# Optimization experiments

Measured on AMD Instinct MI355X. Metric: run time of the kernel, lower is better.

The kernel has to match this reference:

```python
import jax, jax.numpy as jnp
import numpy as np

N_NODES = 50000
GAMMA = -0.5
ZETA = 1.1
DEBUG_VAR = 1e-07


def setup_inputs() -> dict:
    key = jax.random.key(0)
    ks = jax.random.split(key, 8)
    N, E, D, H = N_NODES, 800000, 256, 128
    s = 0.05
    return {
        "x": jax.random.normal(ks[0], (N, D), jnp.float32),
        "W_nb": jax.random.normal(ks[1], (D, H), jnp.float32) * s,
        "b_nb": jnp.zeros((H,), jnp.float32),
        "W_self": jax.random.normal(ks[2], (D, H), jnp.float32) * s,
        "b_self": jnp.zeros((H,), jnp.float32),
        "W_att": jax.random.normal(ks[3], (2 * H, 1), jnp.float32) * s,
        "b_att": jnp.zeros((1,), jnp.float32),
        "values": jax.random.uniform(ks[4], (E,), jnp.float32),
        "noise": jax.random.uniform(ks[5], (E, 1), jnp.float32),
        "row": jax.random.randint(ks[6], (E,), 0, N, jnp.int32),
        "col": jax.random.randint(ks[7], (E,), 0, N, jnp.int32),
    }


def reference(x, W_nb, b_nb, W_self, b_self, W_att, b_att, values, noise, row, col):
    # edge gather + tiny attention MLP
    f1 = jax.nn.relu(x[row] @ W_nb + b_nb)      # [E, H]
    f2 = jax.nn.relu(x[col] @ W_self + b_self)  # [E, H]
    log_alpha = jnp.concatenate([f1, f2], axis=1) @ W_att + b_att  # [E, 1]

    # hard-concrete sample (training=True), beta=1.0
    u = noise + DEBUG_VAR
    gate = jax.nn.sigmoid(jnp.log(u) - jnp.log(1.0 - u) + log_alpha)
    mask = jnp.clip(gate * (ZETA - GAMMA) + GAMMA, 0.0, 1.0)[:, 0]  # [E]

    masked_values = values * mask

    # degree-normalized scatter: rowsum then symmetric D^{-1/2} A D^{-1/2}
    rowsum = jax.ops.segment_sum(masked_values, row, num_segments=N_NODES) + 1e-10
    d_inv_sqrt = jnp.power(rowsum, -0.5)
    d_inv_sqrt = jnp.where(jnp.isinf(d_inv_sqrt), 0.0, d_inv_sqrt)

    norm_values = masked_values * d_inv_sqrt[row] * d_inv_sqrt[col]  # [E]
    return norm_values
```

## Files before the change

kernel.cpp:

```cpp
#include <hip/hip_runtime.h>
#include <hip/hip_bf16.h>

typedef __attribute__((ext_vector_type(8))) short bf16x8;
typedef __attribute__((ext_vector_type(4))) float f32x4;

#define D_DIM 256
#define H_DIM 128
#define QSH 12544
#define NSL 64
#define NMAXL (4 * QSH)

__device__ inline ushort f2bf(float f) {
    union { float f; unsigned u; } a; a.f = f;
    unsigned r = a.u + 0x7fffu + ((a.u >> 16) & 1u);
    return (ushort)(r >> 16);
}
__device__ inline float bf2f(unsigned hi16) {
    union { unsigned u; float f; } a; a.u = hi16 << 16;
    return a.f;
}

__global__ void k0_init(const float* __restrict__ W_nb, const float* __restrict__ W_self,
                        ushort* __restrict__ Wt, float* __restrict__ dis, int N, int init_dis) {
    int i = blockIdx.x * 256 + threadIdx.x;
    if (i < 2 * H_DIM * D_DIM) {
        int j    = i & 7;
        int lane = (i >> 3) & 63;
        int ks   = (i >> 9) & 7;
        int ni   = (i >> 12) & 3;
        int cg   = i >> 14;
        int li   = lane & 15;
        int grp  = lane >> 4;
        int h    = (cg & 1) * 64 + ni * 16 + li;
        int k    = ks * 32 + grp * 8 + j;
        const float* W = (cg >> 1) ? W_self : W_nb;
        Wt[i] = f2bf(W[k * H_DIM + h]);
    }
    if (init_dis && i < N) dis[i] = 1e-10f;
}

__global__ __launch_bounds__(512, 2) void k1_gemm(
    const float* __restrict__ x, const ushort* __restrict__ Wt,
    const float* __restrict__ b_nb, const float* __restrict__ b_self,
    const float* __restrict__ W_att,
    float* __restrict__ g_nb, float* __restrict__ g_self, int N, int ntiles)
{
    __shared__ __align__(16) ushort A_lds[64][264];
    __shared__ float part[2][2][64];

    const int t    = threadIdx.x;
    const int lane = t & 63;
    const int w    = t >> 6;
    const int rh   = w >> 2;
    const int cg   = w & 3;
    const int br   = cg >> 1;
    const int ch   = cg & 1;
    const int li   = lane & 15;
    const int grp  = lane >> 4;

    float bias[4], aw[4];
    #pragma unroll
    for (int ni = 0; ni < 4; ni++) {
        int hh = ch * 64 + ni * 16 + li;
        bias[ni] = br ? b_self[hh] : b_nb[hh];
        aw[ni]   = W_att[br * H_DIM + hh];
    }

    bf16x8 Bf[4][8];
    #pragma unroll
    for (int ni = 0; ni < 4; ni++)
        #pragma unroll
        for (int ks = 0; ks < 8; ks++)
            Bf[ni][ks] = *reinterpret_cast<const bf16x8*>(
                Wt + (((size_t)(cg * 4 + ni) * 8 + ks) << 9) + lane * 8);

    const int sr = t >> 3;
    const int sc = t & 7;

    for (int rt = blockIdx.x; rt < ntiles; rt += gridDim.x) {
        const int row0 = rt * 64;

        __syncthreads();
        {
            const int gr = row0 + sr;
            const bool v = gr < N;
            const float4* src = reinterpret_cast<const float4*>(x + (size_t)gr * D_DIM);
            #pragma unroll
            for (int j = 0; j < 8; j++) {
                int c4 = sc + j * 8;
                ushort4 o;
                if (v) {
                    float4 f = src[c4];
                    o.x = f2bf(f.x); o.y = f2bf(f.y); o.z = f2bf(f.z); o.w = f2bf(f.w);
                } else { o.x = 0; o.y = 0; o.z = 0; o.w = 0; }
                *reinterpret_cast<ushort4*>(&A_lds[sr][c4 * 4]) = o;
            }
        }
        __syncthreads();

        f32x4 acc[2][4];
        #pragma unroll
        for (int mi = 0; mi < 2; mi++)
            #pragma unroll
            for (int ni = 0; ni < 4; ni++) acc[mi][ni] = f32x4{0.f, 0.f, 0.f, 0.f};

        #pragma unroll
        for (int ks = 0; ks < 8; ks++) {
            bf16x8 af0 = *reinterpret_cast<const bf16x8*>(&A_lds[rh * 32 + li][ks * 32 + grp * 8]);
            bf16x8 af1 = *reinterpret_cast<const bf16x8*>(&A_lds[rh * 32 + 16 + li][ks * 32 + grp * 8]);
            #pragma unroll
            for (int ni = 0; ni < 4; ni++) {
                acc[0][ni] = __builtin_amdgcn_mfma_f32_16x16x32_bf16(af0, Bf[ni][ks], acc[0][ni], 0, 0, 0);
                acc[1][ni] = __builtin_amdgcn_mfma_f32_16x16x32_bf16(af1, Bf[ni][ks], acc[1][ni], 0, 0, 0);
            }
        }

        float p[2][4];
        #pragma unroll
        for (int mi = 0; mi < 2; mi++)
            #pragma unroll
            for (int r4 = 0; r4 < 4; r4++) p[mi][r4] = 0.f;
        #pragma unroll
        for (int ni = 0; ni < 4; ni++)
            #pragma unroll
            for (int mi = 0; mi < 2; mi++)
                #pragma unroll
                for (int r4 = 0; r4 < 4; r4++) {
                    float y = acc[mi][ni][r4] + bias[ni];
                    y = y > 0.f ? y : 0.f;
                    p[mi][r4] += y * aw[ni];
                }
        #pragma unroll
        for (int mi = 0; mi < 2; mi++)
            #pragma unroll
            for (int r4 = 0; r4 < 4; r4++) {
                float v = p[mi][r4];
                #pragma unroll
                for (int m = 1; m < 16; m <<= 1) v += __shfl_xor(v, m);
                if (li == 0)
                    part[br][ch][rh * 32 + mi * 16 + grp * 4 + r4] = v;
            }
        __syncthreads();

        if (t < 128) {
            int b_ = t >> 6, lr = t & 63;
            int gr = row0 + lr;
            if (gr < N) {
                float val = part[b_][0][lr] + part[b_][1][lr];
                if (b_) g_self[gr] = val; else g_nb[gr] = val;
            }
        }
    }
}

__global__ __launch_bounds__(256) void k2a_gate(
    const int* __restrict__ row, const int* __restrict__ col,
    const float* __restrict__ values, const float* __restrict__ noise,
    const float* __restrict__ g_nb, const float* __restrict__ g_self,
    const float* __restrict__ b_att, unsigned* __restrict__ pk, int E)
{
    int i = (blockIdx.x * 256 + threadIdx.x) * 4;
    if (i >= E) return;
    const float ba = b_att[0];
    if (i + 3 < E) {
        int4   r4 = *reinterpret_cast<const int4*>(row + i);
        int4   c4 = *reinterpret_cast<const int4*>(col + i);
        float4 v4 = *reinterpret_cast<const float4*>(values + i);
        float4 u4 = *reinterpret_cast<const float4*>(noise + i);
        int   rr[4] = { r4.x, r4.y, r4.z, r4.w };
        int   cc[4] = { c4.x, c4.y, c4.z, c4.w };
        float vv[4] = { v4.x, v4.y, v4.z, v4.w };
        float uu[4] = { u4.x, u4.y, u4.z, u4.w };
        float gn[4], gs[4];
        #pragma unroll
        for (int j = 0; j < 4; j++) { gn[j] = g_nb[rr[j]]; gs[j] = g_self[cc[j]]; }
        unsigned pkv[4];
        #pragma unroll
        for (int j = 0; j < 4; j++) {
            float u    = uu[j] + 1e-7f;
            float la   = gn[j] + gs[j] + ba;
            float gate = u / (u + (1.f - u) * __expf(-la));
            float mask = fminf(fmaxf(gate * 1.6f - 0.5f, 0.f), 1.f);
            pkv[j] = ((unsigned)rr[j] << 16) | (unsigned)f2bf(vv[j] * mask);
        }
        *reinterpret_cast<uint4*>(pk + i) = make_uint4(pkv[0], pkv[1], pkv[2], pkv[3]);
    } else {
        for (int j = 0; j < 4 && i + j < E; j++) {
            int e = i + j;
            int   r = row[e];
            float u    = noise[e] + 1e-7f;
            float la   = g_nb[r] + g_self[col[e]] + ba;
            float gate = u / (u + (1.f - u) * __expf(-la));
            float mask = fminf(fmaxf(gate * 1.6f - 0.5f, 0.f), 1.f);
            pk[e] = ((unsigned)r << 16) | (unsigned)f2bf(values[e] * mask);
        }
    }
}

__global__ __launch_bounds__(1024) void k2q_scatter(
    const unsigned* __restrict__ pk, ushort* __restrict__ priv, int E, int ES)
{
    __shared__ float acc[QSH];
    const int s  = blockIdx.x >> 2;
    const int q  = blockIdx.x & 3;
    const int t  = threadIdx.x;
    const int lo = q * QSH;

    for (int i = t; i < QSH; i += 1024) acc[i] = 0.f;
    __syncthreads();

    const int base = s * ES;
    int end = base + ES; if (end > E) end = E;

    int i = base + t * 4;
    for (; i + 3 < end; i += 4096) {
        uint4 p4 = *reinterpret_cast<const uint4*>(pk + i);
        unsigned p; int d; float m;
        p = p4.x; d = (int)(p >> 16) - lo; m = bf2f(p & 0xffffu);
        if ((unsigned)d < (unsigned)QSH && m != 0.f) atomicAdd(&acc[d], m);
        p = p4.y; d = (int)(p >> 16) - lo; m = bf2f(p & 0xffffu);
        if ((unsigned)d < (unsigned)QSH && m != 0.f) atomicAdd(&acc[d], m);
        p = p4.z; d = (int)(p >> 16) - lo; m = bf2f(p & 0xffffu);
        if ((unsigned)d < (unsigned)QSH && m != 0.f) atomicAdd(&acc[d], m);
        p = p4.w; d = (int)(p >> 16) - lo; m = bf2f(p & 0xffffu);
        if ((unsigned)d < (unsigned)QSH && m != 0.f) atomicAdd(&acc[d], m);
    }
    for (; i < end; i++) {
        unsigned p = pk[i];
        int d = (int)(p >> 16) - lo;
        float m = bf2f(p & 0xffffu);
        if ((unsigned)d < (unsigned)QSH && m != 0.f) atomicAdd(&acc[d], m);
    }
    __syncthreads();

    ushort* dst = priv + (size_t)s * (4 * QSH) + lo;
    for (int j = t * 2; j < QSH; j += 2048) {
        unsigned pkk = (unsigned)f2bf(acc[j]) | ((unsigned)f2bf(acc[j + 1]) << 16);
        *reinterpret_cast<unsigned*>(dst + j) = pkk;
    }
}

__global__ __launch_bounds__(256) void k2c_reduce(
    const ushort* __restrict__ priv, ushort* __restrict__ disb, int N)
{
    int n0 = (blockIdx.x * 256 + threadIdx.x) * 2;
    if (n0 >= N) return;
    float s0 = 1e-10f, s1 = 1e-10f;
    for (int p = 0; p < NSL; p++) {
        unsigned v = *reinterpret_cast<const unsigned*>(priv + (size_t)p * (4 * QSH) + n0);
        s0 += bf2f(v & 0xffffu);
        s1 += bf2f(v >> 16);
    }
    unsigned o = (unsigned)f2bf(rsqrtf(s0)) | ((unsigned)f2bf(rsqrtf(s1)) << 16);
    *reinterpret_cast<unsigned*>(disb + n0) = o;
}

__global__ __launch_bounds__(1024) void k3_edge2_lds(
    const unsigned* __restrict__ pk, const int* __restrict__ col,
    float* __restrict__ out, const ushort* __restrict__ disb,
    int Npad2, int E, int EB)
{
    __shared__ ushort ldis[NMAXL];
    const int t = threadIdx.x;
    {
        const unsigned* src = reinterpret_cast<const unsigned*>(disb);
        unsigned* dst = reinterpret_cast<unsigned*>(ldis);
        const int nw = Npad2 >> 1;
        for (int i = t; i < nw; i += 1024) dst[i] = src[i];
    }
    __syncthreads();

    const int base = blockIdx.x * EB;
    int end = base + EB; if (end > E) end = E;

    int i = base + t * 4;
    for (; i + 3 < end; i += 4096) {
        uint4 p4 = *reinterpret_cast<const uint4*>(pk + i);
        int4  c4 = *reinterpret_cast<const int4*>(col + i);
        float4 o;
        o.x = bf2f(p4.x & 0xffffu) * bf2f(ldis[p4.x >> 16]) * bf2f(ldis[c4.x]);
        o.y = bf2f(p4.y & 0xffffu) * bf2f(ldis[p4.y >> 16]) * bf2f(ldis[c4.y]);
        o.z = bf2f(p4.z & 0xffffu) * bf2f(ldis[p4.z >> 16]) * bf2f(ldis[c4.z]);
        o.w = bf2f(p4.w & 0xffffu) * bf2f(ldis[p4.w >> 16]) * bf2f(ldis[c4.w]);
        *reinterpret_cast<float4*>(out + i) = o;
    }
    for (; i < end; i++) {
        unsigned p = pk[i];
        out[i] = bf2f(p & 0xffffu) * bf2f(ldis[p >> 16]) * bf2f(ldis[col[i]]);
    }
}

__global__ __launch_bounds__(256) void k2_atomic_fb(
    const int* __restrict__ row, const int* __restrict__ col,
    const float* __restrict__ values, const float* __restrict__ noise,
    const float* __restrict__ g_nb, const float* __restrict__ g_self,
    const float* __restrict__ b_att,
    float* __restrict__ out, float* __restrict__ dis, int E)
{
    int e = blockIdx.x * 256 + threadIdx.x;
    if (e >= E) return;
    int   r = row[e], c = col[e];
    float u = noise[e] + 1e-7f;
    float la = g_nb[r] + g_self[c] + b_att[0];
    float gate = u / (u + (1.f - u) * __expf(-la));
    float mask = fminf(fmaxf(gate * 1.6f - 0.5f, 0.f), 1.f);
    float m = values[e] * mask;
    out[e] = m;
    if (m != 0.f) atomicAdd(&dis[r], m);
}
__global__ __launch_bounds__(256) void k2c_rsqrt_fb(float* __restrict__ dis, int N)
{
    int n = blockIdx.x * 256 + threadIdx.x;
    if (n < N) dis[n] = rsqrtf(dis[n]);
}
__global__ __launch_bounds__(256) void k3_edge2_fb(
    const int* __restrict__ row, const int* __restrict__ col,
    float* __restrict__ out, const float* __restrict__ dis, int E)
{
    int e = blockIdx.x * 256 + threadIdx.x;
    if (e >= E) return;
    out[e] = out[e] * dis[row[e]] * dis[col[e]];
}

extern "C" void kernel_launch(void* const* d_in, const int* in_sizes, int n_in,
                              void* d_out, int out_size, void* d_ws, size_t ws_size,
                              hipStream_t stream) {
    const float* x      = (const float*)d_in[0];
    const float* W_nb   = (const float*)d_in[1];
    const float* b_nb   = (const float*)d_in[2];
    const float* W_self = (const float*)d_in[3];
    const float* b_self = (const float*)d_in[4];
    const float* W_att  = (const float*)d_in[5];
    const float* b_att  = (const float*)d_in[6];
    const float* values = (const float*)d_in[7];
    const float* noise  = (const float*)d_in[8];
    const int*   row    = (const int*)d_in[9];
    const int*   col    = (const int*)d_in[10];

    const int N = in_sizes[0] / D_DIM;
    const int E = in_sizes[7];
    float* out = (float*)d_out;

    char* ws = (char*)d_ws;
    ushort* Wt     = (ushort*)ws;
    float*  g_nb   = (float*)(ws + 131072);
    float*  g_self = g_nb + N;
    float*  dis    = g_self + N;
    ushort* disb   = (ushort*)dis;
    ushort* priv   = (ushort*)(dis + N);
    size_t pk_off  = 131072 + (size_t)3 * N * 4 + (size_t)NSL * NMAXL * 2;
    pk_off = (pk_off + 15) & ~(size_t)15;
    unsigned* pk   = (unsigned*)(ws + pk_off);

    const int Npad2 = (N + 1) & ~1;
    int ES = ((E + NSL - 1) / NSL + 3) & ~3;
    size_t need = pk_off + (size_t)E * 4;
    bool lds_path = (N <= NMAXL) && (need <= ws_size);

    int init_n = 2 * H_DIM * D_DIM;
    if (N > init_n) init_n = N;
    k0_init<<<(init_n + 255) / 256, 256, 0, stream>>>(W_nb, W_self, Wt, dis, N, lds_path ? 0 : 1);

    const int ntiles = (N + 63) / 64;
    k1_gemm<<<256, 512, 0, stream>>>(x, Wt, b_nb, b_self, W_att, g_nb, g_self, N, ntiles);

    if (lds_path) {
        int eb4 = ((E + 3) / 4 + 255) / 256;
        k2a_gate<<<eb4, 256, 0, stream>>>(row, col, values, noise, g_nb, g_self,
                                          b_att, pk, E);
        k2q_scatter<<<NSL * 4, 1024, 0, stream>>>(pk, priv, E, ES);
        k2c_reduce<<<((N + 1) / 2 + 255) / 256, 256, 0, stream>>>(priv, disb, N);
        int EB = ((E + 255) / 256 + 3) & ~3;
        k3_edge2_lds<<<256, 1024, 0, stream>>>(pk, col, out, disb, Npad2, E, EB);
    } else {
        k2_atomic_fb<<<(E + 255) / 256, 256, 0, stream>>>(row, col, values, noise,
                                                          g_nb, g_self, b_att, out, dis, E);
        k2c_rsqrt_fb<<<(N + 255) / 256, 256, 0, stream>>>(dis, N);
        k3_edge2_fb<<<(E + 255) / 256, 256, 0, stream>>>(row, col, out, dis, E);
    }
}
```

Measured before the change: 58.05 us.

## Load GEMM A-fragments directly from global into registers, drop LDS staging

The node GEMM kernel stops staging 64-row tiles of x into shared memory. Each of four waves now loads its own 16-row fragment straight from global memory into registers, converting to bf16 on the fly. Tiles shrink to 16 rows, blocks to 256 threads, and the grid grows to 512 blocks. This removes the LDS write/read and one barrier per tile. In exchange, all four waves read the same x rows (redundant global/L2 traffic), and each lane's loads are strided 32-byte chunks that coalesce less well.

Measured after the change: 64.48 us. 1.11x slower.

```diff
diff --git a/kernel.cpp b/kernel.cpp
--- a/kernel.cpp
+++ b/kernel.cpp
@@ -39,20 +39,17 @@
     if (init_dis && i < N) dis[i] = 1e-10f;
 }
 
-__global__ __launch_bounds__(512, 2) void k1_gemm(
+__global__ __launch_bounds__(256, 2) void k1_gemm(
     const float* __restrict__ x, const ushort* __restrict__ Wt,
     const float* __restrict__ b_nb, const float* __restrict__ b_self,
     const float* __restrict__ W_att,
     float* __restrict__ g_nb, float* __restrict__ g_self, int N, int ntiles)
 {
-    __shared__ __align__(16) ushort A_lds[64][264];
-    __shared__ float part[2][2][64];
+    __shared__ float part[4][16];
 
     const int t    = threadIdx.x;
     const int lane = t & 63;
-    const int w    = t >> 6;
-    const int rh   = w >> 2;
-    const int cg   = w & 3;
+    const int cg   = t >> 6;
     const int br   = cg >> 1;
     const int ch   = cg & 1;
     const int li   = lane & 15;
@@ -74,82 +71,66 @@
             Bf[ni][ks] = *reinterpret_cast<const bf16x8*>(
                 Wt + (((size_t)(cg * 4 + ni) * 8 + ks) << 9) + lane * 8);
 
-    const int sr = t >> 3;
-    const int sc = t & 7;
-
     for (int rt = blockIdx.x; rt < ntiles; rt += gridDim.x) {
-        const int row0 = rt * 64;
-
-        __syncthreads();
-        {
-            const int gr = row0 + sr;
-            const bool v = gr < N;
-            const float4* src = reinterpret_cast<const float4*>(x + (size_t)gr * D_DIM);
+        const int row0 = rt * 16;
+        const int gr   = row0 + li;
+        const bool v   = gr < N;
+        const float* xr = x + (size_t)gr * D_DIM + grp * 8;
+
+        union { bf16x8 v8; ushort u[8]; } af[8];
+        #pragma unroll
+        for (int ks = 0; ks < 8; ks++) {
+            float4 a0, a1;
+            if (v) {
+                a0 = *reinterpret_cast<const float4*>(xr + ks * 32);
+                a1 = *reinterpret_cast<const float4*>(xr + ks * 32 + 4);
+            } else {
+                a0 = make_float4(0.f, 0.f, 0.f, 0.f);
+                a1 = a0;
+            }
+            af[ks].u[0] = f2bf(a0.x); af[ks].u[1] = f2bf(a0.y);
+            af[ks].u[2] = f2bf(a0.z); af[ks].u[3] = f2bf(a0.w);
+            af[ks].u[4] = f2bf(a1.x); af[ks].u[5] = f2bf(a1.y);
+            af[ks].u[6] = f2bf(a1.z); af[ks].u[7] = f2bf(a1.w);
+        }
+
+        f32x4 acc[4];
+        #pragma unroll
+        for (int ni = 0; ni < 4; ni++) acc[ni] = f32x4{0.f, 0.f, 0.f, 0.f};
+        #pragma unroll
+        for (int ks = 0; ks < 8; ks++)
             #pragma unroll
-            for (int j = 0; j < 8; j++) {
-                int c4 = sc + j * 8;
-                ushort4 o;
-                if (v) {
-                    float4 f = src[c4];
-                    o.x = f2bf(f.x); o.y = f2bf(f.y); o.z = f2bf(f.z); o.w = f2bf(f.w);
-                } else { o.x = 0; o.y = 0; o.z = 0; o.w = 0; }
-                *reinterpret_cast<ushort4*>(&A_lds[sr][c4 * 4]) = o;
-            }
-        }
-        __syncthreads();
-
-        f32x4 acc[2][4];
-        #pragma unroll
-        for (int mi = 0; mi < 2; mi++)
-            #pragma unroll
-            for (int ni = 0; ni < 4; ni++) acc[mi][ni] = f32x4{0.f, 0.f, 0.f, 0.f};
-
-        #pragma unroll
-        for (int ks = 0; ks < 8; ks++) {
-            bf16x8 af0 = *reinterpret_cast<const bf16x8*>(&A_lds[rh * 32 + li][ks * 32 + grp * 8]);
-            bf16x8 af1 = *reinterpret_cast<const bf16x8*>(&A_lds[rh * 32 + 16 + li][ks * 32 + grp * 8]);
+            for (int ni = 0; ni < 4; ni++)
+                acc[ni] = __builtin_amdgcn_mfma_f32_16x16x32_bf16(af[ks].v8, Bf[ni][ks], acc[ni], 0, 0, 0);
+
+        float p[4];
+        #pragma unroll
+        for (int r4 = 0; r4 < 4; r4++) {
+            float s = 0.f;
             #pragma unroll
             for (int ni = 0; ni < 4; ni++) {
-                acc[0][ni] = __builtin_amdgcn_mfma_f32_16x16x32_bf16(af0, Bf[ni][ks], acc[0][ni], 0, 0, 0);
-                acc[1][ni] = __builtin_amdgcn_mfma_f32_16x16x32_bf16(af1, Bf[ni][ks], acc[1][ni], 0, 0, 0);
+                float y = acc[ni][r4] + bias[ni];
+                y = y > 0.f ? y : 0.f;
+                s += y * aw[ni];
             }
-        }
-
-        float p[2][4];
-        #pragma unroll
-        for (int mi = 0; mi < 2; mi++)
             #pragma unroll
-            for (int r4 = 0; r4 < 4; r4++) p[mi][r4] = 0.f;
-        #pragma unroll
-        for (int ni = 0; ni < 4; ni++)
+            for (int m = 1; m < 16; m <<= 1) s += __shfl_xor(s, m);
+            p[r4] = s;
+        }
+        if (li == 0) {
             #pragma unroll
-            for (int mi = 0; mi < 2; mi++)
-                #pragma unroll
-                for (int r4 = 0; r4 < 4; r4++) {
-                    float y = acc[mi][ni][r4] + bias[ni];
-                    y = y > 0.f ? y : 0.f;
-                    p[mi][r4] += y * aw[ni];
-                }
-        #pragma unroll
-        for (int mi = 0; mi < 2; mi++)
-            #pragma unroll
-            for (int r4 = 0; r4 < 4; r4++) {
-                float v = p[mi][r4];
-                #pragma unroll
-                for (int m = 1; m < 16; m <<= 1) v += __shfl_xor(v, m);
-                if (li == 0)
-                    part[br][ch][rh * 32 + mi * 16 + grp * 4 + r4] = v;
+            for (int r4 = 0; r4 < 4; r4++) part[cg][grp * 4 + r4] = p[r4];
+        }
+        __syncthreads();
+        if (t < 32) {
+            int node = t & 15, b_ = t >> 4;
+            int g2 = row0 + node;
+            if (g2 < N) {
+                float val = part[b_ * 2][node] + part[b_ * 2 + 1][node];
+                if (b_) g_self[g2] = val; else g_nb[g2] = val;
             }
+        }
         __syncthreads();
-
-        if (t < 128) {
-            int b_ = t >> 6, lr = t & 63;
-            int gr = row0 + lr;
-            if (gr < N) {
-                float val = part[b_][0][lr] + part[b_][1][lr];
-                if (b_) g_self[gr] = val; else g_nb[gr] = val;
-            }
-        }
     }
 }
 
@@ -361,8 +342,9 @@
     if (N > init_n) init_n = N;
     k0_init<<<(init_n + 255) / 256, 256, 0, stream>>>(W_nb, W_self, Wt, dis, N, lds_path ? 0 : 1);
 
-    const int ntiles = (N + 63) / 64;
-    k1_gemm<<<256, 512, 0, stream>>>(x, Wt, b_nb, b_self, W_att, g_nb, g_self, N, ntiles);
+    const int ntiles16 = (N + 15) / 16;
+    int k1grid = ntiles16 < 512 ? ntiles16 : 512;
+    k1_gemm<<<k1grid, 256, 0, stream>>>(x, Wt, b_nb, b_self, W_att, g_nb, g_self, N, ntiles16);
 
     if (lds_path) {
         int eb4 = ((E + 3) / 4 + 255) / 256;
```

## Pre-convert x to MFMA-swizzled bf16 and stage weights in LDS for GEMM

Applied to the files above, without the earlier changes.

The init kernel now also converts x to bf16, writing it in a layout that lets each lane load its MFMA A-fragments straight from global memory. A new GEMM kernel keeps one branch's transposed weights in XOR-swizzled LDS, splits the nb and self branches across alternating blocks, and computes 32-row tiles without staging x through LDS. The aim is to cut the per-tile LDS staging, conversion and barrier cost in the GEMM. The price is an extra bf16 copy of x written to and re-read from global memory (and read by both branch blocks), plus a larger workspace requirement.

New measurement: 67.30 us. +15.9%, slower.

```diff
diff --git a/kernel.cpp b/kernel.cpp
--- a/kernel.cpp
+++ b/kernel.cpp
@@ -20,26 +20,134 @@
     return a.f;
 }
 
-__global__ void k0_init(const float* __restrict__ W_nb, const float* __restrict__ W_self,
-                        ushort* __restrict__ Wt, float* __restrict__ dis, int N, int init_dis) {
+__global__ void k0_init(const float* __restrict__ x,
+                        const float* __restrict__ W_nb, const float* __restrict__ W_self,
+                        ushort* __restrict__ Wt, ushort* __restrict__ xbf,
+                        float* __restrict__ dis, int N, int init_dis, int do_xbf) {
     int i = blockIdx.x * 256 + threadIdx.x;
+    if (do_xbf && i < N * 32) {
+        int n     = i >> 5;
+        int kbase = (i & 31) * 8;
+        const float4* s = reinterpret_cast<const float4*>(x + (size_t)n * D_DIM + kbase);
+        float4 a = s[0], b = s[1];
+        uint4 o;
+        o.x = (unsigned)f2bf(a.x) | ((unsigned)f2bf(a.y) << 16);
+        o.y = (unsigned)f2bf(a.z) | ((unsigned)f2bf(a.w) << 16);
+        o.z = (unsigned)f2bf(b.x) | ((unsigned)f2bf(b.y) << 16);
+        o.w = (unsigned)f2bf(b.z) | ((unsigned)f2bf(b.w) << 16);
+        int T    = n >> 4;
+        int ks   = (i >> 2) & 7;
+        int l    = (i & 3) * 16 + (n & 15);
+        size_t word = ((size_t)T * 8 + ks) * 64 + l;
+        *reinterpret_cast<uint4*>(xbf + word * 8) = o;
+    }
     if (i < 2 * H_DIM * D_DIM) {
-        int j    = i & 7;
-        int lane = (i >> 3) & 63;
-        int ks   = (i >> 9) & 7;
-        int ni   = (i >> 12) & 3;
-        int cg   = i >> 14;
-        int li   = lane & 15;
-        int grp  = lane >> 4;
-        int h    = (cg & 1) * 64 + ni * 16 + li;
-        int k    = ks * 32 + grp * 8 + j;
-        const float* W = (cg >> 1) ? W_self : W_nb;
-        Wt[i] = f2bf(W[k * H_DIM + h]);
+        int sel = i >> 15;
+        int r   = i & 32767;
+        int k   = r >> 7;
+        int h   = r & 127;
+        const float* W = sel ? W_self : W_nb;
+        Wt[(sel * H_DIM + h) * D_DIM + k] = f2bf(W[k * H_DIM + h]);
     }
     if (init_dis && i < N) dis[i] = 1e-10f;
 }
 
-__global__ __launch_bounds__(512, 2) void k1_gemm(
+__global__ __launch_bounds__(256, 2) void k1_ldsb(
+    const ushort* __restrict__ xbf, const ushort* __restrict__ Wt,
+    const float* __restrict__ b_nb, const float* __restrict__ b_self,
+    const float* __restrict__ W_att,
+    float* __restrict__ g_nb, float* __restrict__ g_self,
+    int N, int nt16, int nt32)
+{
+    __shared__ ushort Bl[128 * 256];
+    __shared__ float part[4][32];
+
+    const int t    = threadIdx.x;
+    const int lane = t & 63;
+    const int w    = t >> 6;
+    const int li   = lane & 15;
+    const int grp  = lane >> 4;
+    const int cls  = blockIdx.x & 1;
+
+    {
+        const ushort* Wtg = Wt + (size_t)cls * H_DIM * D_DIM;
+        for (int q = t; q < 4096; q += 256) {
+            int row = q >> 5, c = q & 31;
+            uint4 v = *reinterpret_cast<const uint4*>(Wtg + row * 256 + c * 8);
+            *reinterpret_cast<uint4*>(&Bl[row * 256 + ((c ^ (row & 31)) << 3)]) = v;
+        }
+    }
+
+    float bias[2], aw[2];
+    #pragma unroll
+    for (int ni2 = 0; ni2 < 2; ni2++) {
+        int hl = w * 32 + ni2 * 16 + li;
+        bias[ni2] = cls ? b_self[hl] : b_nb[hl];
+        aw[ni2]   = W_att[cls * H_DIM + hl];
+    }
+    __syncthreads();
+
+    const int G  = gridDim.x >> 1;
+    const int r0 = w * 32 + li;
+    const int r1 = r0 + 16;
+
+    for (int T = blockIdx.x >> 1; T < nt32; T += G) {
+        bf16x8 af[2][8];
+        #pragma unroll
+        for (int mi = 0; mi < 2; mi++) {
+            int t16 = 2 * T + mi;
+            if (t16 < nt16) {
+                #pragma unroll
+                for (int ks = 0; ks < 8; ks++)
+                    af[mi][ks] = *reinterpret_cast<const bf16x8*>(
+                        xbf + (((size_t)t16 * 8 + ks) * 64 + lane) * 8);
+            } else {
+                #pragma unroll
+                for (int ks = 0; ks < 8; ks++) af[mi][ks] = bf16x8{0,0,0,0,0,0,0,0};
+            }
+        }
+
+        f32x4 acc[2][2];
+        #pragma unroll
+        for (int mi = 0; mi < 2; mi++)
+            #pragma unroll
+            for (int ni2 = 0; ni2 < 2; ni2++) acc[mi][ni2] = f32x4{0.f, 0.f, 0.f, 0.f};
+
+        #pragma unroll
+        for (int ks = 0; ks < 8; ks++) {
+            int c = ks * 4 + grp;
+            bf16x8 b0 = *reinterpret_cast<const bf16x8*>(&Bl[r0 * 256 + ((c ^ (r0 & 31)) << 3)]);
+            bf16x8 b1 = *reinterpret_cast<const bf16x8*>(&Bl[r1 * 256 + ((c ^ (r1 & 31)) << 3)]);
+            acc[0][0] = __builtin_amdgcn_mfma_f32_16x16x32_bf16(af[0][ks], b0, acc[0][0], 0, 0, 0);
+            acc[1][0] = __builtin_amdgcn_mfma_f32_16x16x32_bf16(af[1][ks], b0, acc[1][0], 0, 0, 0);
+            acc[0][1] = __builtin_amdgcn_mfma_f32_16x16x32_bf16(af[0][ks], b1, acc[0][1], 0, 0, 0);
+            acc[1][1] = __builtin_amdgcn_mfma_f32_16x16x32_bf16(af[1][ks], b1, acc[1][1], 0, 0, 0);
+        }
+
+        #pragma unroll
+        for (int mi = 0; mi < 2; mi++)
+            #pragma unroll
+            for (int r4 = 0; r4 < 4; r4++) {
+                float y0 = acc[mi][0][r4] + bias[0];
+                float y1 = acc[mi][1][r4] + bias[1];
+                y0 = y0 > 0.f ? y0 : 0.f;
+                y1 = y1 > 0.f ? y1 : 0.f;
+                float s = y0 * aw[0] + y1 * aw[1];
+                #pragma unroll
+                for (int m = 1; m < 16; m <<= 1) s += __shfl_xor(s, m);
+                if (li == 0) part[w][mi * 16 + grp * 4 + r4] = s;
+            }
+        __syncthreads();
+        if (t < 32) {
+            float val = part[0][t] + part[1][t] + part[2][t] + part[3][t];
+            int ng = T * 32 + t;
+            if (ng < N) (cls ? g_self : g_nb)[ng] = val;
+        }
+        __syncthreads();
+    }
+}
+
+__global__ __launch_bounds__(512, 2) void k1_gemm_f(
     const float* __restrict__ x, const ushort* __restrict__ Wt,
     const float* __restrict__ b_nb, const float* __restrict__ b_self,
     const float* __restrict__ W_att,
@@ -72,14 +180,13 @@
         #pragma unroll
         for (int ks = 0; ks < 8; ks++)
             Bf[ni][ks] = *reinterpret_cast<const bf16x8*>(
-                Wt + (((size_t)(cg * 4 + ni) * 8 + ks) << 9) + lane * 8);
+                Wt + (size_t)(cg * 64 + ni * 16 + li) * D_DIM + ks * 32 + grp * 8);
 
     const int sr = t >> 3;
     const int sc = t & 7;
 
     for (int rt = blockIdx.x; rt < ntiles; rt += gridDim.x) {
         const int row0 = rt * 64;
-
         __syncthreads();
         {
             const int gr = row0 + sr;
@@ -351,18 +458,32 @@
     size_t pk_off  = 131072 + (size_t)3 * N * 4 + (size_t)NSL * NMAXL * 2;
     pk_off = (pk_off + 15) & ~(size_t)15;
     unsigned* pk   = (unsigned*)(ws + pk_off);
+    size_t xbf_off = pk_off + (size_t)E * 4;
+    xbf_off = (xbf_off + 15) & ~(size_t)15;
+    ushort* xbf    = (ushort*)(ws + xbf_off);
 
     const int Npad2 = (N + 1) & ~1;
+    const int nt16  = (N + 15) / 16;
+    const int nt32  = (nt16 + 1) / 2;
     int ES = ((E + NSL - 1) / NSL + 3) & ~3;
     size_t need = pk_off + (size_t)E * 4;
     bool lds_path = (N <= NMAXL) && (need <= ws_size);
-
-    int init_n = 2 * H_DIM * D_DIM;
-    if (N > init_n) init_n = N;
-    k0_init<<<(init_n + 255) / 256, 256, 0, stream>>>(W_nb, W_self, Wt, dis, N, lds_path ? 0 : 1);
-
-    const int ntiles = (N + 63) / 64;
-    k1_gemm<<<256, 512, 0, stream>>>(x, Wt, b_nb, b_self, W_att, g_nb, g_self, N, ntiles);
+    bool xbf_path = (xbf_off + (size_t)nt16 * 4096 * 2 <= ws_size);
+
+    int work0 = 2 * H_DIM * D_DIM;
+    if (N > work0) work0 = N;
+    if (xbf_path && N * 32 > work0) work0 = N * 32;
+    k0_init<<<(work0 + 255) / 256, 256, 0, stream>>>(x, W_nb, W_self, Wt, xbf, dis,
+                                                     N, lds_path ? 0 : 1, xbf_path ? 1 : 0);
+
+    if (xbf_path) {
+        int gpairs = nt32 < 256 ? nt32 : 256;
+        k1_ldsb<<<gpairs * 2, 256, 0, stream>>>(xbf, Wt, b_nb, b_self, W_att,
+                                                g_nb, g_self, N, nt16, nt32);
+    } else {
+        const int nt64 = (N + 63) / 64;
+        k1_gemm_f<<<256, 512, 0, stream>>>(x, Wt, b_nb, b_self, W_att, g_nb, g_self, N, nt64);
+    }
 
     if (lds_path) {
         int eb4 = ((E + 3) / 4 + 255) / 256;
```

## Repartition node GEMM warps across columns and double the grid size

Applied to the files above, without the earlier changes.

Each of the 8 warps now owns all 64 rows and a 32-column slice of one branch, instead of half the rows and 64 columns. This halves the per-warp B fragment registers and spreads the attention reduction over four partial sums per branch. The grid grows from 256 to up to 512 blocks so more blocks run at once. In exchange, each warp reads 4 A fragments per k-step from LDS instead of 2, which raises LDS traffic.

Result: slower. 62.66 us (+7.9%).

```diff
diff --git a/kernel.cpp b/kernel.cpp
--- a/kernel.cpp
+++ b/kernel.cpp
@@ -39,40 +39,37 @@
     if (init_dis && i < N) dis[i] = 1e-10f;
 }
 
-__global__ __launch_bounds__(512, 2) void k1_gemm(
+__global__ __launch_bounds__(512, 2) void k1_gemm8(
     const float* __restrict__ x, const ushort* __restrict__ Wt,
     const float* __restrict__ b_nb, const float* __restrict__ b_self,
     const float* __restrict__ W_att,
     float* __restrict__ g_nb, float* __restrict__ g_self, int N, int ntiles)
 {
     __shared__ __align__(16) ushort A_lds[64][264];
-    __shared__ float part[2][2][64];
+    __shared__ float part[8][64];
 
     const int t    = threadIdx.x;
     const int lane = t & 63;
     const int w    = t >> 6;
-    const int rh   = w >> 2;
-    const int cg   = w & 3;
-    const int br   = cg >> 1;
-    const int ch   = cg & 1;
+    const int br   = w >> 2;
     const int li   = lane & 15;
     const int grp  = lane >> 4;
 
-    float bias[4], aw[4];
+    float bias[2], aw[2];
     #pragma unroll
-    for (int ni = 0; ni < 4; ni++) {
-        int hh = ch * 64 + ni * 16 + li;
-        bias[ni] = br ? b_self[hh] : b_nb[hh];
-        aw[ni]   = W_att[br * H_DIM + hh];
-    }
-
-    bf16x8 Bf[4][8];
+    for (int ni2 = 0; ni2 < 2; ni2++) {
+        int hh = (w & 3) * 32 + ni2 * 16 + li;
+        bias[ni2] = br ? b_self[hh] : b_nb[hh];
+        aw[ni2]   = W_att[br * H_DIM + hh];
+    }
+
+    bf16x8 Bf[2][8];
     #pragma unroll
-    for (int ni = 0; ni < 4; ni++)
+    for (int ni2 = 0; ni2 < 2; ni2++)
         #pragma unroll
         for (int ks = 0; ks < 8; ks++)
-            Bf[ni][ks] = *reinterpret_cast<const bf16x8*>(
-                Wt + (((size_t)(cg * 4 + ni) * 8 + ks) << 9) + lane * 8);
+            Bf[ni2][ks] = *reinterpret_cast<const bf16x8*>(
+                Wt + (((size_t)(w * 2 + ni2) * 8 + ks) << 9) + lane * 8);
 
     const int sr = t >> 3;
     const int sc = t & 7;
@@ -98,47 +95,35 @@
         }
         __syncthreads();
 
-        f32x4 acc[2][4];
-        #pragma unroll
-        for (int mi = 0; mi < 2; mi++)
+        f32x4 acc[4][2];
+        #pragma unroll
+        for (int mi = 0; mi < 4; mi++)
             #pragma unroll
-            for (int ni = 0; ni < 4; ni++) acc[mi][ni] = f32x4{0.f, 0.f, 0.f, 0.f};
+            for (int ni2 = 0; ni2 < 2; ni2++) acc[mi][ni2] = f32x4{0.f, 0.f, 0.f, 0.f};
 
         #pragma unroll
         for (int ks = 0; ks < 8; ks++) {
-            bf16x8 af0 = *reinterpret_cast<const bf16x8*>(&A_lds[rh * 32 + li][ks * 32 + grp * 8]);
-            bf16x8 af1 = *reinterpret_cast<const bf16x8*>(&A_lds[rh * 32 + 16 + li][ks * 32 + grp * 8]);
             #pragma unroll
-            for (int ni = 0; ni < 4; ni++) {
-                acc[0][ni] = __builtin_amdgcn_mfma_f32_16x16x32_bf16(af0, Bf[ni][ks], acc[0][ni], 0, 0, 0);
-                acc[1][ni] = __builtin_amdgcn_mfma_f32_16x16x32_bf16(af1, Bf[ni][ks], acc[1][ni], 0, 0, 0);
+            for (int mi = 0; mi < 4; mi++) {
+                bf16x8 af = *reinterpret_cast<const bf16x8*>(
+                    &A_lds[mi * 16 + li][ks * 32 + grp * 8]);
+                acc[mi][0] = __builtin_amdgcn_mfma_f32_16x16x32_bf16(af, Bf[0][ks], acc[mi][0], 0, 0, 0);
+                acc[mi][1] = __builtin_amdgcn_mfma_f32_16x16x32_bf16(af, Bf[1][ks], acc[mi][1], 0, 0, 0);
             }
         }
 
-        float p[2][4];
-        #pragma unroll
-        for (int mi = 0; mi < 2; mi++)
-            #pragma unroll
-            for (int r4 = 0; r4 < 4; r4++) p[mi][r4] = 0.f;
-        #pragma unroll
-        for (int ni = 0; ni < 4; ni++)
-            #pragma unroll
-            for (int mi = 0; mi < 2; mi++)
-                #pragma unroll
-                for (int r4 = 0; r4 < 4; r4++) {
-                    float y = acc[mi][ni][r4] + bias[ni];
-                    y = y > 0.f ? y : 0.f;
-                    p[mi][r4] += y * aw[ni];
-                }
-        #pragma unroll
-        for (int mi = 0; mi < 2; mi++)
+        #pragma unroll
+        for (int mi = 0; mi < 4; mi++)
             #pragma unroll
             for (int r4 = 0; r4 < 4; r4++) {
-                float v = p[mi][r4];
+                float y0 = acc[mi][0][r4] + bias[0];
+                float y1 = acc[mi][1][r4] + bias[1];
+                y0 = y0 > 0.f ? y0 : 0.f;
+                y1 = y1 > 0.f ? y1 : 0.f;
+                float s = y0 * aw[0] + y1 * aw[1];
                 #pragma unroll
-                for (int m = 1; m < 16; m <<= 1) v += __shfl_xor(v, m);
-                if (li == 0)
-                    part[br][ch][rh * 32 + mi * 16 + grp * 4 + r4] = v;
+                for (int m = 1; m < 16; m <<= 1) s += __shfl_xor(s, m);
+                if (li == 0) part[w][mi * 16 + grp * 4 + r4] = s;
             }
         __syncthreads();
 
@@ -146,7 +131,8 @@
             int b_ = t >> 6, lr = t & 63;
             int gr = row0 + lr;
             if (gr < N) {
-                float val = part[b_][0][lr] + part[b_][1][lr];
+                float val = part[b_ * 4 + 0][lr] + part[b_ * 4 + 1][lr]
+                          + part[b_ * 4 + 2][lr] + part[b_ * 4 + 3][lr];
                 if (b_) g_self[gr] = val; else g_nb[gr] = val;
             }
         }
@@ -362,7 +348,8 @@
     k0_init<<<(init_n + 255) / 256, 256, 0, stream>>>(W_nb, W_self, Wt, dis, N, lds_path ? 0 : 1);
 
     const int ntiles = (N + 63) / 64;
-    k1_gemm<<<256, 512, 0, stream>>>(x, Wt, b_nb, b_self, W_att, g_nb, g_self, N, ntiles);
+    int k1grid = ntiles < 512 ? ntiles : 512;
+    k1_gemm8<<<k1grid, 512, 0, stream>>>(x, Wt, b_nb, b_self, W_att, g_nb, g_self, N, ntiles);
 
     if (lds_path) {
         int eb4 = ((E + 3) / 4 + 255) / 256;
```
